# Kernel optimization log

Hardware: AMD Instinct MI355X
Metric: run time of the kernel (lower is better)

The kernel has to match this reference:

```python
import jax, jax.numpy as jnp
import numpy as np

B, IN, OUT = 2048, 256, 256

def setup_inputs() -> dict:
    key = jax.random.key(0)
    k1, k2, k3 = jax.random.split(key, 3)
    x = jax.random.normal(k1, (B, IN), dtype=jnp.float32)
    weight = jax.random.normal(k2, (OUT, IN + 1), dtype=jnp.float32)
    w = jax.random.normal(k3, (OUT, IN + 1), dtype=jnp.float32)
    return {"x": x, "weight": weight, "w": w}

def reference(x, weight, w):
    # append bias column of ones: [B, IN+1]
    x_ext = jnp.concatenate([x, jnp.ones((x.shape[0], 1), dtype=x.dtype)], axis=1)
    # y[b,o] = sum_i weight[o,i] * sin(w[o,i] * x_ext[b,i])
    # broadcast to [B, OUT, IN+1], fused sin+mul, reduce over i
    y = jnp.sum(weight[None, :, :] * jnp.sin(w[None, :, :] * x_ext[:, None, :]), axis=2)
    return y
```

## Files before the change

### kernel.cpp

```cpp
#include <hip/hip_runtime.h>


#define IN_DIM 256
#define OUT_DIM 256
#define LDW 257
#define LXS 65
#define INV_2PI 0.15915494309189535f

__global__ __launch_bounds__(256, 4)
void skan_kernel(const float* __restrict__ x,
                 const float* __restrict__ weight,
                 const float* __restrict__ wfreq,
                 float* __restrict__ y)
{
    __shared__ float lx[64 * LXS];

    const int t  = threadIdx.x;
    const int l  = t & 63;
    const int wv = __builtin_amdgcn_readfirstlane(t >> 6);

    const int obase = (blockIdx.x & 31) * 8;
    const int b0    = (blockIdx.x >> 5) * 64;

    const int o0 = obase + wv * 2;
    const int o1 = o0 + 1;
    const float* __restrict__ w0r = wfreq  + o0 * LDW;
    const float* __restrict__ g0r = weight + o0 * LDW;
    const float* __restrict__ w1r = wfreq  + o1 * LDW;
    const float* __restrict__ g1r = weight + o1 * LDW;

    const int srow = wv * 16 + (l >> 4);
    const int scol = (l & 15) * 4;

    float acc0 = g0r[IN_DIM] * __builtin_amdgcn_sinf(w0r[IN_DIM] * INV_2PI);
    float acc1 = g1r[IN_DIM] * __builtin_amdgcn_sinf(w1r[IN_DIM] * INV_2PI);

    {
        const float* gx = x + b0 * IN_DIM;
#pragma unroll
        for (int k = 0; k < 4; ++k) {
            const int r = srow + 4 * k;
            const float4 v = *(const float4*)(gx + r * IN_DIM + scol);
            float* d = &lx[r * LXS + scol];
            d[0] = v.x * INV_2PI; d[1] = v.y * INV_2PI;
            d[2] = v.z * INV_2PI; d[3] = v.w * INV_2PI;
        }
    }

    for (int ic = 0; ic < 4; ++ic) {
        __syncthreads();

        float xs[64];
#pragma unroll
        for (int j = 0; j < 64; ++j) xs[j] = lx[l * LXS + j];

        __syncthreads();

        if (ic < 3) {
            const float* gx = x + b0 * IN_DIM + (ic + 1) * 64;
#pragma unroll
            for (int k = 0; k < 4; ++k) {
                const int r = srow + 4 * k;
                const float4 v = *(const float4*)(gx + r * IN_DIM + scol);
                float* d = &lx[r * LXS + scol];
                d[0] = v.x * INV_2PI; d[1] = v.y * INV_2PI;
                d[2] = v.z * INV_2PI; d[3] = v.w * INV_2PI;
            }
        }

        const int ib = ic * 64;
#pragma unroll
        for (int j = 0; j < 64; ++j) {
            const float xv = xs[j];
            acc0 = fmaf(g0r[ib + j], __builtin_amdgcn_sinf(w0r[ib + j] * xv), acc0);
            acc1 = fmaf(g1r[ib + j], __builtin_amdgcn_sinf(w1r[ib + j] * xv), acc1);
        }
    }

    y[(b0 + l) * OUT_DIM + o0] = acc0;
    y[(b0 + l) * OUT_DIM + o1] = acc1;
}

extern "C" void kernel_launch(void* const* d_in, const int* in_sizes, int n_in,
                              void* d_out, int out_size, void* d_ws, size_t ws_size,
                              hipStream_t stream) {
    const float* x      = (const float*)d_in[0];
    const float* weight = (const float*)d_in[1];
    const float* wfreq  = (const float*)d_in[2];
    float* y            = (float*)d_out;

    const int B = in_sizes[0] / IN_DIM;
    const int grid = (B / 64) * (OUT_DIM / 8);

    skan_kernel<<<grid, 256, 0, stream>>>(x, weight, wfreq, y);
}
```

Measured before the change: 76.24 us.

## Double-buffer x and stage interleaved weight/frequency rows in LDS per chunk

Measured after the change: 78.48 us. +2.9%, slower.

```diff
diff --git a/kernel.cpp b/kernel.cpp
--- a/kernel.cpp
+++ b/kernel.cpp
@@ -4,7 +4,10 @@
 #define IN_DIM 256
 #define OUT_DIM 256
 #define LDW 257
-#define LXS 65
+#define CHUNK 32
+#define NCHUNK 8
+#define LXS 33
+#define WGS 20
 #define INV_2PI 0.15915494309189535f
 
 __global__ __launch_bounds__(256, 4)
@@ -13,7 +16,8 @@
                  const float* __restrict__ wfreq,
                  float* __restrict__ y)
 {
-    __shared__ float lx[64 * LXS];
+    __shared__ __align__(16) float lx[2][64 * LXS];
+    __shared__ __align__(16) float wg[2][CHUNK * WGS];
 
     const int t  = threadIdx.x;
     const int l  = t & 63;
@@ -23,62 +27,66 @@
     const int b0    = (blockIdx.x >> 5) * 64;
 
     const int o0 = obase + wv * 2;
-    const int o1 = o0 + 1;
-    const float* __restrict__ w0r = wfreq  + o0 * LDW;
-    const float* __restrict__ g0r = weight + o0 * LDW;
-    const float* __restrict__ w1r = wfreq  + o1 * LDW;
-    const float* __restrict__ g1r = weight + o1 * LDW;
 
-    const int srow = wv * 16 + (l >> 4);
-    const int scol = (l & 15) * 4;
-
+    const float* w0r = wfreq  + o0 * LDW;
+    const float* g0r = weight + o0 * LDW;
+    const float* w1r = wfreq  + (o0 + 1) * LDW;
+    const float* g1r = weight + (o0 + 1) * LDW;
     float acc0 = g0r[IN_DIM] * __builtin_amdgcn_sinf(w0r[IN_DIM] * INV_2PI);
     float acc1 = g1r[IN_DIM] * __builtin_amdgcn_sinf(w1r[IN_DIM] * INV_2PI);
 
+    const int xr = t >> 2;
+    const int xc = (t & 3) * 8;
+    const float* xrow = x + (b0 + xr) * IN_DIM + xc;
+    const int so = t >> 5;
+    const int sj = t & 31;
+    const float* wsrc = wfreq  + (obase + so) * LDW + sj;
+    const float* gsrc = weight + (obase + so) * LDW + sj;
+    const int wslot = sj * WGS + (so >> 1) * 4 + (so & 1) * 2;
+
     {
-        const float* gx = x + b0 * IN_DIM;
+        const float4 a = *(const float4*)(xrow + 0);
+        const float4 b = *(const float4*)(xrow + 4);
+        float* d = &lx[0][xr * LXS + xc];
+        d[0] = a.x * INV_2PI; d[1] = a.y * INV_2PI;
+        d[2] = a.z * INV_2PI; d[3] = a.w * INV_2PI;
+        d[4] = b.x * INV_2PI; d[5] = b.y * INV_2PI;
+        d[6] = b.z * INV_2PI; d[7] = b.w * INV_2PI;
+        wg[0][wslot]     = wsrc[0];
+        wg[0][wslot + 1] = gsrc[0];
+    }
+
+    for (int c = 0; c < NCHUNK; ++c) {
+        __syncthreads();
+        const int cur = c & 1;
+
+        if (c + 1 < NCHUNK) {
+            const int nxt = cur ^ 1;
+            const int off = (c + 1) * CHUNK;
+            const float4 a = *(const float4*)(xrow + off);
+            const float4 b = *(const float4*)(xrow + off + 4);
+            float* d = &lx[nxt][xr * LXS + xc];
+            d[0] = a.x * INV_2PI; d[1] = a.y * INV_2PI;
+            d[2] = a.z * INV_2PI; d[3] = a.w * INV_2PI;
+            d[4] = b.x * INV_2PI; d[5] = b.y * INV_2PI;
+            d[6] = b.z * INV_2PI; d[7] = b.w * INV_2PI;
+            wg[nxt][wslot]     = wsrc[off];
+            wg[nxt][wslot + 1] = gsrc[off];
+        }
+
+        const float* lxr = &lx[cur][l * LXS];
+        const float* wgr = &wg[cur][wv * 4];
 #pragma unroll
-        for (int k = 0; k < 4; ++k) {
-            const int r = srow + 4 * k;
-            const float4 v = *(const float4*)(gx + r * IN_DIM + scol);
-            float* d = &lx[r * LXS + scol];
-            d[0] = v.x * INV_2PI; d[1] = v.y * INV_2PI;
-            d[2] = v.z * INV_2PI; d[3] = v.w * INV_2PI;
+        for (int j = 0; j < CHUNK; ++j) {
+            const float4 f = *(const float4*)(wgr + j * WGS);
+            const float xv = lxr[j];
+            acc0 = fmaf(f.y, __builtin_amdgcn_sinf(f.x * xv), acc0);
+            acc1 = fmaf(f.w, __builtin_amdgcn_sinf(f.z * xv), acc1);
         }
     }
 
-    for (int ic = 0; ic < 4; ++ic) {
-        __syncthreads();
-
-        float xs[64];
-#pragma unroll
-        for (int j = 0; j < 64; ++j) xs[j] = lx[l * LXS + j];
-
-        __syncthreads();
-
-        if (ic < 3) {
-            const float* gx = x + b0 * IN_DIM + (ic + 1) * 64;
-#pragma unroll
-            for (int k = 0; k < 4; ++k) {
-                const int r = srow + 4 * k;
-                const float4 v = *(const float4*)(gx + r * IN_DIM + scol);
-                float* d = &lx[r * LXS + scol];
-                d[0] = v.x * INV_2PI; d[1] = v.y * INV_2PI;
-                d[2] = v.z * INV_2PI; d[3] = v.w * INV_2PI;
-            }
-        }
-
-        const int ib = ic * 64;
-#pragma unroll
-        for (int j = 0; j < 64; ++j) {
-            const float xv = xs[j];
-            acc0 = fmaf(g0r[ib + j], __builtin_amdgcn_sinf(w0r[ib + j] * xv), acc0);
-            acc1 = fmaf(g1r[ib + j], __builtin_amdgcn_sinf(w1r[ib + j] * xv), acc1);
-        }
-    }
-
-    y[(b0 + l) * OUT_DIM + o0] = acc0;
-    y[(b0 + l) * OUT_DIM + o1] = acc1;
+    y[(b0 + l) * OUT_DIM + o0]     = acc0;
+    y[(b0 + l) * OUT_DIM + o0 + 1] = acc1;
 }
 
 extern "C" void kernel_launch(void* const* d_in, const int* in_sizes, int n_in,
```

## Cache weight slices in registers and split input dim across lanes with DPP reduce

Applied to the files above, without the earlier changes.

New measurement: 77.31 us. Within noise of the previous version (+1.4%).

```diff
diff --git a/kernel.cpp b/kernel.cpp
--- a/kernel.cpp
+++ b/kernel.cpp
@@ -4,8 +4,17 @@
 #define IN_DIM 256
 #define OUT_DIM 256
 #define LDW 257
-#define LXS 65
 #define INV_2PI 0.15915494309189535f
+#define BTILE 32
+#define NBG (BTILE / 4)
+#define SLOT 20
+
+template <int CTRL>
+__device__ __forceinline__ float ror_add(float v) {
+    const int m = __builtin_amdgcn_update_dpp(0, __float_as_int(v),
+                                              CTRL, 0xf, 0xf, true);
+    return v + __int_as_float(m);
+}
 
 __global__ __launch_bounds__(256, 4)
 void skan_kernel(const float* __restrict__ x,
@@ -13,72 +22,78 @@
                  const float* __restrict__ wfreq,
                  float* __restrict__ y)
 {
-    __shared__ float lx[64 * LXS];
+    __shared__ __align__(16) float lxT[2][4 * 16 * SLOT];
 
-    const int t  = threadIdx.x;
-    const int l  = t & 63;
-    const int wv = __builtin_amdgcn_readfirstlane(t >> 6);
+    const int t    = threadIdx.x;
+    const int l    = t & 63;
+    const int wv   = t >> 6;
+    const int isub = l & 15;
+    const int bsub = l >> 4;
 
     const int obase = (blockIdx.x & 31) * 8;
-    const int b0    = (blockIdx.x >> 5) * 64;
+    const int b0    = (blockIdx.x >> 5) * BTILE;
+    const int o0    = obase + wv * 2;
 
-    const int o0 = obase + wv * 2;
-    const int o1 = o0 + 1;
-    const float* __restrict__ w0r = wfreq  + o0 * LDW;
-    const float* __restrict__ g0r = weight + o0 * LDW;
-    const float* __restrict__ w1r = wfreq  + o1 * LDW;
-    const float* __restrict__ g1r = weight + o1 * LDW;
+    float wc0[16], gc0[16], wc1[16], gc1[16];
+    {
+        const float* wp = wfreq  + o0 * LDW + isub * 16;
+        const float* gp = weight + o0 * LDW + isub * 16;
+#pragma unroll
+        for (int j = 0; j < 16; ++j) {
+            wc0[j] = wp[j]       * INV_2PI;
+            gc0[j] = gp[j];
+            wc1[j] = wp[LDW + j] * INV_2PI;
+            gc1[j] = gp[LDW + j];
+        }
+    }
+    const float bias0 = weight[o0 * LDW + IN_DIM] *
+                        __builtin_amdgcn_sinf(wfreq[o0 * LDW + IN_DIM] * INV_2PI);
+    const float bias1 = weight[(o0 + 1) * LDW + IN_DIM] *
+                        __builtin_amdgcn_sinf(wfreq[(o0 + 1) * LDW + IN_DIM] * INV_2PI);
 
-    const int srow = wv * 16 + (l >> 4);
-    const int scol = (l & 15) * 4;
-
-    float acc0 = g0r[IN_DIM] * __builtin_amdgcn_sinf(w0r[IN_DIM] * INV_2PI);
-    float acc1 = g1r[IN_DIM] * __builtin_amdgcn_sinf(w1r[IN_DIM] * INV_2PI);
+    const int    srow = t >> 6;
+    const float* xsrc = x + (b0 + srow) * IN_DIM + (t & 63) * 4;
+    const int    dsto = (srow * 16 + ((t & 63) >> 2)) * SLOT + (t & 3) * 4;
+    const int    rdo  = (bsub * 16 + isub) * SLOT;
 
     {
-        const float* gx = x + b0 * IN_DIM;
+        const float4 v = *(const float4*)xsrc;
+        *(float4*)&lxT[0][dsto] = v;
+    }
+
+    for (int bg = 0; bg < NBG; ++bg) {
+        __syncthreads();
+        const int cur = bg & 1;
+
+        float xv[16];
+        *(float4*)&xv[0]  = *(const float4*)&lxT[cur][rdo + 0];
+        *(float4*)&xv[4]  = *(const float4*)&lxT[cur][rdo + 4];
+        *(float4*)&xv[8]  = *(const float4*)&lxT[cur][rdo + 8];
+        *(float4*)&xv[12] = *(const float4*)&lxT[cur][rdo + 12];
+
+        float4 nx;
+        if (bg + 1 < NBG) nx = *(const float4*)(xsrc + (bg + 1) * 4 * IN_DIM);
+
+        float a0 = 0.f, a1 = 0.f;
 #pragma unroll
-        for (int k = 0; k < 4; ++k) {
-            const int r = srow + 4 * k;
-            const float4 v = *(const float4*)(gx + r * IN_DIM + scol);
-            float* d = &lx[r * LXS + scol];
-            d[0] = v.x * INV_2PI; d[1] = v.y * INV_2PI;
-            d[2] = v.z * INV_2PI; d[3] = v.w * INV_2PI;
+        for (int j = 0; j < 16; ++j) {
+            const float xj = xv[j];
+            a0 = fmaf(gc0[j], __builtin_amdgcn_sinf(wc0[j] * xj), a0);
+            a1 = fmaf(gc1[j], __builtin_amdgcn_sinf(wc1[j] * xj), a1);
+        }
+
+        if (bg + 1 < NBG) *(float4*)&lxT[cur ^ 1][dsto] = nx;
+
+        a0 = ror_add<0x121>(a0); a0 = ror_add<0x122>(a0);
+        a0 = ror_add<0x124>(a0); a0 = ror_add<0x128>(a0);
+        a1 = ror_add<0x121>(a1); a1 = ror_add<0x122>(a1);
+        a1 = ror_add<0x124>(a1); a1 = ror_add<0x128>(a1);
+
+        if (isub < 2) {
+            const float out = (isub == 0) ? a0 + bias0 : a1 + bias1;
+            y[(b0 + bg * 4 + bsub) * OUT_DIM + o0 + isub] = out;
         }
     }
-
-    for (int ic = 0; ic < 4; ++ic) {
-        __syncthreads();
-
-        float xs[64];
-#pragma unroll
-        for (int j = 0; j < 64; ++j) xs[j] = lx[l * LXS + j];
-
-        __syncthreads();
-
-        if (ic < 3) {
-            const float* gx = x + b0 * IN_DIM + (ic + 1) * 64;
-#pragma unroll
-            for (int k = 0; k < 4; ++k) {
-                const int r = srow + 4 * k;
-                const float4 v = *(const float4*)(gx + r * IN_DIM + scol);
-                float* d = &lx[r * LXS + scol];
-                d[0] = v.x * INV_2PI; d[1] = v.y * INV_2PI;
-                d[2] = v.z * INV_2PI; d[3] = v.w * INV_2PI;
-            }
-        }
-
-        const int ib = ic * 64;
-#pragma unroll
-        for (int j = 0; j < 64; ++j) {
-            const float xv = xs[j];
-            acc0 = fmaf(g0r[ib + j], __builtin_amdgcn_sinf(w0r[ib + j] * xv), acc0);
-            acc1 = fmaf(g1r[ib + j], __builtin_amdgcn_sinf(w1r[ib + j] * xv), acc1);
-        }
-    }
-
-    y[(b0 + l) * OUT_DIM + o0] = acc0;
-    y[(b0 + l) * OUT_DIM + o1] = acc1;
 }
 
 extern "C" void kernel_launch(void* const* d_in, const int* in_sizes, int n_in,
@@ -90,7 +105,7 @@
     float* y            = (float*)d_out;
 
     const int B = in_sizes[0] / IN_DIM;
-    const int grid = (B / 64) * (OUT_DIM / 8);
+    const int grid = (B / BTILE) * (OUT_DIM / 8);
 
     skan_kernel<<<grid, 256, 0, stream>>>(x, weight, wfreq, y);
 }
```
